# Kernel optimization log

Hardware: AMD Instinct MI355X
Metric: run time of the kernel (lower is better)

Reference implementation:

```python
import jax, jax.numpy as jnp
import numpy as np
from jax import lax

DIM = 384
HEADS = 8
HEAD_DIM = DIM // HEADS
MLP_HIDDEN = int(DIM * 4.0)
B, Hs, Ws = 32, 56, 56
N = Hs * Ws


def layernorm(x, w, b, eps=1e-5):
    mu = jnp.mean(x, axis=-1, keepdims=True)
    var = jnp.mean(jnp.square(x - mu), axis=-1, keepdims=True)
    return (x - mu) * lax.rsqrt(var + eps) * w + b


def setup_inputs() -> dict:
    key = jax.random.key(0)
    ks = jax.random.split(key, 16)
    s = 0.02
    inp = {
        "x": jax.random.normal(ks[0], (B, N, DIM), jnp.float32),
        "H": Hs,
        "W": Ws,
        # CPE depthwise 3x3 conv (groups=dim) -> OIHW kernel [C,1,3,3]
        "cpe_w": jax.random.normal(ks[1], (DIM, 1, 3, 3), jnp.float32) * s,
        "cpe_b": jnp.zeros((DIM,), jnp.float32),
        "ln1_w": jnp.ones((DIM,), jnp.float32),
        "ln1_b": jnp.zeros((DIM,), jnp.float32),
        "qkv_w": jax.random.normal(ks[2], (3 * DIM, DIM), jnp.float32) * s,
        "qkv_b": jnp.zeros((3 * DIM,), jnp.float32),
        "temperature": jnp.ones((HEADS, 1, 1), jnp.float32) * (HEAD_DIM ** -0.5),
        "proj_w": jax.random.normal(ks[3], (DIM, DIM), jnp.float32) * s,
        "proj_b": jnp.zeros((DIM,), jnp.float32),
        "ln2_w": jnp.ones((DIM,), jnp.float32),
        "ln2_b": jnp.zeros((DIM,), jnp.float32),
        "fc1_w": jax.random.normal(ks[4], (MLP_HIDDEN, DIM), jnp.float32) * s,
        "fc1_b": jnp.zeros((MLP_HIDDEN,), jnp.float32),
        "fc2_w": jax.random.normal(ks[5], (DIM, MLP_HIDDEN), jnp.float32) * s,
        "fc2_b": jnp.zeros((DIM,), jnp.float32),
    }
    return inp


def reference(x, H, W, cpe_w, cpe_b, ln1_w, ln1_b, qkv_w, qkv_b, temperature,
              proj_w, proj_b, ln2_w, ln2_b, fc1_w, fc1_b, fc2_w, fc2_b):
    Bn, Nn, C = x.shape
    # --- CPE: depthwise 3x3 conv residual (identity activation, cpe_act=False) ---
    feat = x.transpose(0, 2, 1).reshape(Bn, C, H, W)
    feat = lax.conv_general_dilated(
        feat, cpe_w, window_strides=(1, 1), padding="SAME",
        feature_group_count=C, dimension_numbers=("NCHW", "OIHW", "NCHW"))
    feat = feat + cpe_b[None, :, None, None]
    x = x + feat.reshape(Bn, C, Nn).transpose(0, 2, 1)

    # --- linear attention ---
    cur = layernorm(x, ln1_w, ln1_b)
    qkv = cur @ qkv_w.T + qkv_b                      # [B,N,3C]
    qkv = qkv.reshape(Bn, Nn, 3, HEADS, HEAD_DIM).transpose(2, 0, 3, 1, 4)
    q, k, v = qkv[0], qkv[1], qkv[2]                 # [B,h,N,d]
    q = jax.nn.relu(q)
    k = jax.nn.relu(k)
    k_sum = jnp.sum(k, axis=2)                       # [B,h,d]
    denom = jnp.maximum(jnp.einsum("bhnd,bhd->bhn", q, k_sum)[..., None], 100.0)
    kv = jnp.einsum("bhnd,bhne->bhde", k, v) * temperature  # [B,h,d,d]
    attn_out = jnp.einsum("bhnd,bhde->bhne", q, kv) / denom  # [B,h,N,d]
    attn_out = attn_out.transpose(0, 2, 1, 3).reshape(Bn, Nn, C)
    attn_out = attn_out @ proj_w.T + proj_b
    x = x + attn_out

    # --- MLP residual ---
    cur = layernorm(x, ln2_w, ln2_b)
    h = jax.nn.gelu(cur @ fc1_w.T + fc1_b, approximate=False)
    x = x + (h @ fc2_w.T + fc2_b)
    return x


if __name__ == "__main__":
    out = reference(**setup_inputs())
    print(out.shape, out.dtype)
```

## Files before the change

kernel.cpp:

```cpp
#include <hip/hip_runtime.h>
#include <hip/hip_bf16.h>
#include <math.h>

#define BDIM 384
#define HEADS 8
#define HD 48
#define HID 1536
#define BB 32
#define HH 56
#define WW 56
#define NN 3136
#define MTOT (BB*NN)
#define TPW 8

typedef unsigned short ushort_t;
typedef __attribute__((ext_vector_type(8))) short short8;
typedef __attribute__((ext_vector_type(4))) float floatx4;

__device__ inline float bf2f(ushort_t u){ return __uint_as_float(((unsigned)u)<<16); }
__device__ inline ushort_t f2bf(float f){
  unsigned u = __float_as_uint(f);
  u += 0x7fff + ((u>>16)&1);
  return (ushort_t)(u>>16);
}

__device__ inline void async_ld16(const void* g, void* l){
  __builtin_amdgcn_global_load_lds((const __attribute__((address_space(1))) void*)g,
                                   (__attribute__((address_space(3))) void*)l, 16, 0, 0);
}

__global__ void convert_bf16_kernel(const float* __restrict__ in, ushort_t* __restrict__ out, int n){
  int i = blockIdx.x*256 + threadIdx.x;
  if (i < n) out[i] = f2bf(in[i]);
}

__global__ __launch_bounds__(256)
void cpe_ln1_kernel(const float* __restrict__ x, const float* __restrict__ cw,
                    const float* __restrict__ cb, const float* __restrict__ lw,
                    const float* __restrict__ lb, float* __restrict__ x1out,
                    ushort_t* __restrict__ cur){
  int lane = threadIdx.x & 63, wave = threadIdx.x >> 6;
  size_t base = ((size_t)blockIdx.x*4 + wave) * TPW;
  float wreg[6][9], cbr[6], lwr[6], lbr[6];
  #pragma unroll
  for (int p = 0; p < 6; ++p){
    int c = p*64 + lane;
    cbr[p] = cb[c]; lwr[p] = lw[c]; lbr[p] = lb[c];
    #pragma unroll
    for (int j = 0; j < 9; ++j) wreg[p][j] = cw[c*9+j];
  }
  for (int ti = 0; ti < TPW; ++ti){
    size_t bn = base + ti;
    int b = (int)(bn / NN), n = (int)(bn % NN);
    int h = n / WW, w = n % WW;
    const float* xb = x + ((size_t)b*NN)*BDIM;
    float conv[6];
    #pragma unroll
    for (int p = 0; p < 6; ++p) conv[p] = cbr[p];
    #pragma unroll
    for (int dh = -1; dh <= 1; ++dh){
      int hh = h + dh; if ((unsigned)hh >= HH) continue;
      #pragma unroll
      for (int dw = -1; dw <= 1; ++dw){
        int w2 = w + dw; if ((unsigned)w2 >= WW) continue;
        const float* src = xb + (size_t)(hh*WW + w2)*BDIM + lane;
        int j = (dh+1)*3 + (dw+1);
        #pragma unroll
        for (int p = 0; p < 6; ++p) conv[p] += src[p*64] * wreg[p][j];
      }
    }
    const float* xc = xb + (size_t)n*BDIM + lane;
    float x1[6], s = 0.f, q = 0.f;
    #pragma unroll
    for (int p = 0; p < 6; ++p){
      x1[p] = xc[p*64] + conv[p];
      s += x1[p]; q += x1[p]*x1[p];
    }
    #pragma unroll
    for (int off = 32; off; off >>= 1){
      s += __shfl_xor(s, off);
      q += __shfl_xor(q, off);
    }
    float mean = s*(1.f/384.f);
    float rstd = rsqrtf(q*(1.f/384.f) - mean*mean + 1e-5f);
    float* xo = x1out + bn*BDIM + lane;
    ushort_t* co = cur + bn*BDIM + lane;
    #pragma unroll
    for (int p = 0; p < 6; ++p){
      xo[p*64] = x1[p];
      co[p*64] = f2bf((x1[p]-mean)*rstd*lwr[p] + lbr[p]);
    }
  }
}

__global__ __launch_bounds__(256)
void ln_kernel(const float* __restrict__ xin, const float* __restrict__ lw,
               const float* __restrict__ lb, ushort_t* __restrict__ outb){
  int lane = threadIdx.x & 63, wave = threadIdx.x >> 6;
  size_t base = ((size_t)blockIdx.x*4 + wave) * TPW;
  float lwr[6], lbr[6];
  #pragma unroll
  for (int p = 0; p < 6; ++p){ lwr[p] = lw[p*64+lane]; lbr[p] = lb[p*64+lane]; }
  for (int ti = 0; ti < TPW; ++ti){
    size_t bn = base + ti;
    const float* xi = xin + bn*BDIM + lane;
    float v[6], s = 0.f, q = 0.f;
    #pragma unroll
    for (int p = 0; p < 6; ++p){
      v[p] = xi[p*64];
      s += v[p]; q += v[p]*v[p];
    }
    #pragma unroll
    for (int off = 32; off; off >>= 1){
      s += __shfl_xor(s, off);
      q += __shfl_xor(q, off);
    }
    float mean = s*(1.f/384.f);
    float rstd = rsqrtf(q*(1.f/384.f) - mean*mean + 1e-5f);
    ushort_t* oo = outb + bn*BDIM + lane;
    #pragma unroll
    for (int p = 0; p < 6; ++p) oo[p*64] = f2bf((v[p]-mean)*rstd*lwr[p] + lbr[p]);
  }
}

template<int EP>
__global__ __launch_bounds__(256)
void gemm_kernel(const ushort_t* __restrict__ A, const ushort_t* __restrict__ Bw,
                 const float* __restrict__ bias, const float* __restrict__ resid,
                 void* __restrict__ outp, int Ncols, int K){
  __shared__ __align__(16) ushort_t As[2*128*32];
  __shared__ __align__(16) ushort_t Bs[2*128*32];
  const int t = threadIdx.x;
  const int lane = t & 63, wave = t >> 6;
  const int wm = wave >> 1, wn = wave & 1;

  const int gx = gridDim.x;
  const int nwg = gx * gridDim.y;
  int orig = blockIdx.y * gx + blockIdx.x;
  int qn = nwg >> 3, rn = nwg & 7;
  int xcd = orig & 7, pos = orig >> 3;
  int wg = (xcd < rn ? xcd*(qn+1) : rn*(qn+1) + (xcd-rn)*qn) + pos;
  int bx = wg % gx;
  int by = wg / gx;

  const size_t m0 = (size_t)by * 128;
  const int n0 = bx * 128;
  const int lrow = lane & 15, lk = (lane >> 4) << 3;
  floatx4 zero4 = {0.f, 0.f, 0.f, 0.f};
  floatx4 acc[4][4];
  #pragma unroll
  for (int i = 0; i < 4; ++i)
    #pragma unroll
    for (int j = 0; j < 4; ++j) acc[i][j] = zero4;

  for (int k0 = 0; k0 < K; k0 += 64){
    #pragma unroll
    for (int l = 0; l < 4; ++l){
      int idx = t + l*256;
      int row = (idx >> 2) & 127;
      int ko  = (idx >> 9)*32 + (idx & 3)*8;
      int lbase = (l*256 + wave*64) * 8;
      async_ld16(&A[(m0 + row)*K + (k0 + ko)], &As[lbase]);
      async_ld16(&Bw[(size_t)(n0 + row)*K + (k0 + ko)], &Bs[lbase]);
    }
    __syncthreads();
    #pragma unroll
    for (int half = 0; half < 2; ++half){
      const ushort_t* Ah = &As[half*4096];
      const ushort_t* Bh = &Bs[half*4096];
      short8 af[4], bfr[4];
      #pragma unroll
      for (int i = 0; i < 4; ++i) af[i]  = *(const short8*)&Ah[(wm*64 + i*16 + lrow)*32 + lk];
      #pragma unroll
      for (int j = 0; j < 4; ++j) bfr[j] = *(const short8*)&Bh[(wn*64 + j*16 + lrow)*32 + lk];
      #pragma unroll
      for (int i = 0; i < 4; ++i)
        #pragma unroll
        for (int j = 0; j < 4; ++j)
          acc[i][j] = __builtin_amdgcn_mfma_f32_16x16x32_bf16(af[i], bfr[j], acc[i][j], 0, 0, 0);
    }
    __syncthreads();
  }

  const int quad = lane >> 4;
  #pragma unroll
  for (int i = 0; i < 4; ++i){
    #pragma unroll
    for (int j = 0; j < 4; ++j){
      int gn = n0 + wn*64 + j*16 + lrow;
      float bv = bias[gn];
      #pragma unroll
      for (int r = 0; r < 4; ++r){
        size_t gm = m0 + wm*64 + i*16 + quad*4 + r;
        float v = acc[i][j][r] + bv;
        if constexpr (EP == 0){
          if (gn < 768) v = fmaxf(v, 0.f);
          ((ushort_t*)outp)[gm*Ncols + gn] = f2bf(v);
        } else if constexpr (EP == 1){
          v = 0.5f*v*(1.f + erff(v*0.70710678118f));
          ((ushort_t*)outp)[gm*Ncols + gn] = f2bf(v);
        } else {
          ((float*)outp)[gm*Ncols + gn] = v + resid[gm*Ncols + gn];
        }
      }
    }
  }
}

__global__ __launch_bounds__(256)
void kv_mfma_kernel(const ushort_t* __restrict__ qkv, float* __restrict__ kvT_out,
                    float* __restrict__ ksum_out){
  __shared__ __align__(16) ushort_t smem[2*48*72];
  ushort_t* kT = smem;
  ushort_t* vT = smem + 48*72;
  int bh = blockIdx.x, b = bh >> 3, h = bh & 7;
  int chunk = blockIdx.y;
  int t = threadIdx.x, lane = t & 63, wave = t >> 6;
  int lrow = lane & 15, quad = lane >> 4;
  const ushort_t* kb = qkv + (size_t)b*NN*1152 + 384 + h*48;
  const ushort_t* vb = kb + 384;
  floatx4 acc[9];
  #pragma unroll
  for (int i = 0; i < 9; ++i) acc[i] = (floatx4){0.f,0.f,0.f,0.f};
  float ks = 0.f;

  for (int s = 0; s < 7; ++s){
    int n0 = chunk*448 + s*64;
    #pragma unroll
    for (int p = 0; p < 3; ++p){
      int u = t + p*256;
      int arr = u / 384;
      int r = u - arr*384;
      int d8 = r >> 6;
      int nl = r & 63;
      const ushort_t* src = (arr ? vb : kb) + (size_t)(n0 + nl)*1152 + d8*8;
      ushort_t* dst = arr ? vT : kT;
      uint4 val = *(const uint4*)src;
      ushort_t tmp[8];
      *(uint4*)tmp = val;
      #pragma unroll
      for (int j = 0; j < 8; ++j) dst[(d8*8 + j)*72 + nl] = tmp[j];
    }
    __syncthreads();
    if ((wave >> 1) == (s & 1)){
      int kloc = (wave & 1) * 32;
      short8 af[3], bfv[3];
      #pragma unroll
      for (int i = 0; i < 3; ++i) af[i]  = *(const short8*)&kT[(i*16 + lrow)*72 + kloc + quad*8];
      #pragma unroll
      for (int j = 0; j < 3; ++j) bfv[j] = *(const short8*)&vT[(j*16 + lrow)*72 + kloc + quad*8];
      #pragma unroll
      for (int i = 0; i < 3; ++i)
        #pragma unroll
        for (int j = 0; j < 3; ++j)
          acc[i*3+j] = __builtin_amdgcn_mfma_f32_16x16x32_bf16(af[i], bfv[j], acc[i*3+j], 0, 0, 0);
    }
    if (wave == 3 && lane < 48){
      float s2 = 0.f;
      #pragma unroll
      for (int q8 = 0; q8 < 8; ++q8){
        short8 kk = *(const short8*)&kT[lane*72 + q8*8];
        #pragma unroll
        for (int j = 0; j < 8; ++j) s2 += bf2f((ushort_t)kk[j]);
      }
      ks += s2;
    }
    __syncthreads();
  }

  float* F = (float*)smem;
  #define DUMP(W) if (wave == (W)){ _Pragma("unroll") for (int ti = 0; ti < 9; ++ti){ _Pragma("unroll") for (int r = 0; r < 4; ++r){ int d = (ti/3)*16 + quad*4 + r, e = (ti%3)*16 + lrow; F[d*48 + e] = acc[ti][r]; } } }
  #define ADDF(W) if (wave == (W)){ _Pragma("unroll") for (int ti = 0; ti < 9; ++ti){ _Pragma("unroll") for (int r = 0; r < 4; ++r){ int d = (ti/3)*16 + quad*4 + r, e = (ti%3)*16 + lrow; acc[ti][r] += F[d*48 + e]; } } }
  DUMP(1) __syncthreads(); ADDF(0) __syncthreads();
  DUMP(3) __syncthreads(); ADDF(2) __syncthreads();
  DUMP(2) __syncthreads(); ADDF(0) __syncthreads();
  #undef DUMP
  #undef ADDF
  if (wave == 0){
    #pragma unroll
    for (int ti = 0; ti < 9; ++ti){
      #pragma unroll
      for (int r = 0; r < 4; ++r){
        int d = (ti/3)*16 + quad*4 + r, e = (ti%3)*16 + lrow;
        atomicAdd(&kvT_out[(size_t)bh*2304 + e*48 + d], acc[ti][r]);
      }
    }
  }
  if (wave == 3 && lane < 48) atomicAdd(&ksum_out[bh*48 + lane], ks);
}

__global__ __launch_bounds__(256)
void attn_mfma_kernel(const ushort_t* __restrict__ qkv, const float* __restrict__ kvT,
                      const float* __restrict__ ksum, const float* __restrict__ temp,
                      ushort_t* __restrict__ attn_out){
  __shared__ __align__(16) ushort_t Bs[64*72];
  int bh = blockIdx.x, b = bh >> 3, h = bh & 7;
  int t = threadIdx.x, lane = t & 63, wave = t >> 6;
  int lrow = lane & 15, quad = lane >> 4;
  float tf = temp[h];
  for (int u = t; u < 64*72; u += 256){
    int col = u / 72, d = u - col*72;
    float v = 0.f;
    if (d < 48){
      if (col < 48) v = kvT[(size_t)bh*2304 + col*48 + d] * tf;
      else if (col == 48) v = ksum[bh*48 + d];
    }
    Bs[u] = f2bf(v);
  }
  __syncthreads();
  short8 bfv[4][2];
  #pragma unroll
  for (int j = 0; j < 4; ++j)
    #pragma unroll
    for (int s = 0; s < 2; ++s)
      bfv[j][s] = *(const short8*)&Bs[(j*16 + lrow)*72 + s*32 + quad*8];

  const ushort_t* qb = qkv + (size_t)b*NN*1152 + h*48;
  int n0 = blockIdx.y*256 + wave*64;
  floatx4 acc[4][4];
  #pragma unroll
  for (int i = 0; i < 4; ++i)
    #pragma unroll
    for (int j = 0; j < 4; ++j) acc[i][j] = (floatx4){0.f,0.f,0.f,0.f};

  #pragma unroll
  for (int i = 0; i < 4; ++i){
    int nrow = n0 + i*16 + lrow;
    #pragma unroll
    for (int s = 0; s < 2; ++s){
      short8 af = *(const short8*)&qb[(size_t)nrow*1152 + s*32 + quad*8];
      #pragma unroll
      for (int j = 0; j < 4; ++j)
        acc[i][j] = __builtin_amdgcn_mfma_f32_16x16x32_bf16(af, bfv[j][s], acc[i][j], 0, 0, 0);
    }
  }

  ushort_t* ob = attn_out + (size_t)b*NN*BDIM + h*48;
  #pragma unroll
  for (int i = 0; i < 4; ++i){
    #pragma unroll
    for (int r = 0; r < 4; ++r){
      float den = __shfl(acc[i][3][r], quad*16);
      den = fmaxf(den, 100.f);
      int nrow = n0 + i*16 + quad*4 + r;
      if (nrow < NN){
        #pragma unroll
        for (int j = 0; j < 3; ++j)
          ob[(size_t)nrow*BDIM + j*16 + lrow] = f2bf(acc[i][j][r] / den);
      }
    }
  }
}

extern "C" void kernel_launch(void* const* d_in, const int* in_sizes, int n_in,
                              void* d_out, int out_size, void* d_ws, size_t ws_size,
                              hipStream_t stream){
  const float* x     = (const float*)d_in[0];
  const float* cpe_w = (const float*)d_in[3];
  const float* cpe_b = (const float*)d_in[4];
  const float* ln1_w = (const float*)d_in[5];
  const float* ln1_b = (const float*)d_in[6];
  const float* qkv_w = (const float*)d_in[7];
  const float* qkv_b = (const float*)d_in[8];
  const float* temp  = (const float*)d_in[9];
  const float* proj_w= (const float*)d_in[10];
  const float* proj_b= (const float*)d_in[11];
  const float* ln2_w = (const float*)d_in[12];
  const float* ln2_b = (const float*)d_in[13];
  const float* fc1_w = (const float*)d_in[14];
  const float* fc1_b = (const float*)d_in[15];
  const float* fc2_w = (const float*)d_in[16];
  const float* fc2_b = (const float*)d_in[17];
  float* out = (float*)d_out;

  char* ws = (char*)d_ws;
  size_t off = 0;
  auto alloc = [&](size_t bytes) -> void* {
    void* p = ws + off;
    off += (bytes + 255) & ~(size_t)255;
    return p;
  };
  ushort_t* cur  = (ushort_t*)alloc((size_t)MTOT*BDIM*2);
  ushort_t* big  = (ushort_t*)alloc((size_t)MTOT*HID*2);
  float*    kvT  = (float*)   alloc((size_t)BB*HEADS*HD*HD*4);
  float*    ksum = (float*)   alloc((size_t)BB*HEADS*HD*4);
  ushort_t* wq = (ushort_t*)alloc((size_t)3*BDIM*BDIM*2);
  ushort_t* wp = (ushort_t*)alloc((size_t)BDIM*BDIM*2);
  ushort_t* w1 = (ushort_t*)alloc((size_t)HID*BDIM*2);
  ushort_t* w2 = (ushort_t*)alloc((size_t)BDIM*HID*2);

  convert_bf16_kernel<<<(3*BDIM*BDIM + 255)/256, 256, 0, stream>>>(qkv_w, wq, 3*BDIM*BDIM);
  convert_bf16_kernel<<<(BDIM*BDIM + 255)/256, 256, 0, stream>>>(proj_w, wp, BDIM*BDIM);
  convert_bf16_kernel<<<(HID*BDIM + 255)/256, 256, 0, stream>>>(fc1_w, w1, HID*BDIM);
  convert_bf16_kernel<<<(BDIM*HID + 255)/256, 256, 0, stream>>>(fc2_w, w2, BDIM*HID);

  hipMemsetAsync(kvT, 0, (size_t)BB*HEADS*HD*HD*4, stream);
  hipMemsetAsync(ksum, 0, (size_t)BB*HEADS*HD*4, stream);

  cpe_ln1_kernel<<<MTOT/(4*TPW), 256, 0, stream>>>(x, cpe_w, cpe_b, ln1_w, ln1_b, out, cur);
  gemm_kernel<0><<<dim3(9, 784), 256, 0, stream>>>(cur, wq, qkv_b, nullptr, big, 1152, BDIM);
  kv_mfma_kernel<<<dim3(BB*HEADS, 7), 256, 0, stream>>>(big, kvT, ksum);
  attn_mfma_kernel<<<dim3(BB*HEADS, 13), 256, 0, stream>>>(big, kvT, ksum, temp, cur);
  gemm_kernel<2><<<dim3(3, 784), 256, 0, stream>>>(cur, wp, proj_b, out, out, BDIM, BDIM);
  ln_kernel<<<MTOT/(4*TPW), 256, 0, stream>>>(out, ln2_w, ln2_b, cur);
  gemm_kernel<1><<<dim3(12, 784), 256, 0, stream>>>(cur, w1, fc1_b, nullptr, big, HID, BDIM);
  gemm_kernel<2><<<dim3(3, 784), 256, 0, stream>>>(big, w2, fc2_b, out, out, BDIM, HID);
}
```

Measured before the change: 1.419 ms.

## Enlarge GEMM tile to 256 rows with 512 threads and use fast erf

The GEMM block tile grows from 128x128 to 256x128, using 8 waves and 512 threads, so each weight tile in LDS is shared by twice as many rows and the number of blocks halves. The exact erff in the GELU epilogue is replaced by the Abramowitz-Stegun polynomial approximation built on exp2f, which lowers epilogue arithmetic at a small accuracy cost (max error around 1e-7). The larger tile uses more LDS per block, which may cut occupancy, and it leaves fewer blocks to spread across the CUs.

```diff
diff --git a/kernel.cpp b/kernel.cpp
--- a/kernel.cpp
+++ b/kernel.cpp
@@ -24,6 +24,16 @@
   return (ushort_t)(u>>16);
 }
 
+__device__ inline float erf_fast(float z){
+  float az = fabsf(z);
+  float tt = 1.f/(1.f + 0.3275911f*az);
+  float poly = tt*(0.254829592f + tt*(-0.284496736f + tt*(1.421413741f +
+               tt*(-1.453152027f + tt*1.061405429f))));
+  float e = exp2f(-az*az*1.4426950408889634f);
+  float r = 1.f - poly*e;
+  return copysignf(r, z);
+}
+
 __device__ inline void async_ld16(const void* g, void* l){
   __builtin_amdgcn_global_load_lds((const __attribute__((address_space(1))) void*)g,
                                    (__attribute__((address_space(3))) void*)l, 16, 0, 0);
@@ -124,11 +134,11 @@
 }
 
 template<int EP>
-__global__ __launch_bounds__(256)
+__global__ __launch_bounds__(512)
 void gemm_kernel(const ushort_t* __restrict__ A, const ushort_t* __restrict__ Bw,
                  const float* __restrict__ bias, const float* __restrict__ resid,
                  void* __restrict__ outp, int Ncols, int K){
-  __shared__ __align__(16) ushort_t As[2*128*32];
+  __shared__ __align__(16) ushort_t As[2*256*32];
   __shared__ __align__(16) ushort_t Bs[2*128*32];
   const int t = threadIdx.x;
   const int lane = t & 63, wave = t >> 6;
@@ -143,7 +153,7 @@
   int bx = wg % gx;
   int by = wg / gx;
 
-  const size_t m0 = (size_t)by * 128;
+  const size_t m0 = (size_t)by * 256;
   const int n0 = bx * 128;
   const int lrow = lane & 15, lk = (lane >> 4) << 3;
   floatx4 zero4 = {0.f, 0.f, 0.f, 0.f};
@@ -156,17 +166,21 @@
   for (int k0 = 0; k0 < K; k0 += 64){
     #pragma unroll
     for (int l = 0; l < 4; ++l){
-      int idx = t + l*256;
-      int row = (idx >> 2) & 127;
-      int ko  = (idx >> 9)*32 + (idx & 3)*8;
-      int lbase = (l*256 + wave*64) * 8;
-      async_ld16(&A[(m0 + row)*K + (k0 + ko)], &As[lbase]);
-      async_ld16(&Bw[(size_t)(n0 + row)*K + (k0 + ko)], &Bs[lbase]);
+      int idx = t + l*512;
+      int lbase = (l*512 + wave*64) * 8;
+      int arow = (idx >> 2) & 255;
+      int ako  = (idx >> 10)*32 + (idx & 3)*8;
+      async_ld16(&A[(m0 + arow)*K + (k0 + ako)], &As[lbase]);
+      if (l < 2){
+        int brow = (idx >> 2) & 127;
+        int bko  = (idx >> 9)*32 + (idx & 3)*8;
+        async_ld16(&Bw[(size_t)(n0 + brow)*K + (k0 + bko)], &Bs[lbase]);
+      }
     }
     __syncthreads();
     #pragma unroll
     for (int half = 0; half < 2; ++half){
-      const ushort_t* Ah = &As[half*4096];
+      const ushort_t* Ah = &As[half*8192];
       const ushort_t* Bh = &Bs[half*4096];
       short8 af[4], bfr[4];
       #pragma unroll
@@ -197,7 +211,7 @@
           if (gn < 768) v = fmaxf(v, 0.f);
           ((ushort_t*)outp)[gm*Ncols + gn] = f2bf(v);
         } else if constexpr (EP == 1){
-          v = 0.5f*v*(1.f + erff(v*0.70710678118f));
+          v = 0.5f*v*(1.f + erf_fast(v*0.70710678118f));
           ((ushort_t*)outp)[gm*Ncols + gn] = f2bf(v);
         } else {
           ((float*)outp)[gm*Ncols + gn] = v + resid[gm*Ncols + gn];
@@ -398,11 +412,11 @@
   hipMemsetAsync(ksum, 0, (size_t)BB*HEADS*HD*4, stream);
 
   cpe_ln1_kernel<<<MTOT/(4*TPW), 256, 0, stream>>>(x, cpe_w, cpe_b, ln1_w, ln1_b, out, cur);
-  gemm_kernel<0><<<dim3(9, 784), 256, 0, stream>>>(cur, wq, qkv_b, nullptr, big, 1152, BDIM);
+  gemm_kernel<0><<<dim3(9, MTOT/256), 512, 0, stream>>>(cur, wq, qkv_b, nullptr, big, 1152, BDIM);
   kv_mfma_kernel<<<dim3(BB*HEADS, 7), 256, 0, stream>>>(big, kvT, ksum);
   attn_mfma_kernel<<<dim3(BB*HEADS, 13), 256, 0, stream>>>(big, kvT, ksum, temp, cur);
-  gemm_kernel<2><<<dim3(3, 784), 256, 0, stream>>>(cur, wp, proj_b, out, out, BDIM, BDIM);
+  gemm_kernel<2><<<dim3(3, MTOT/256), 512, 0, stream>>>(cur, wp, proj_b, out, out, BDIM, BDIM);
   ln_kernel<<<MTOT/(4*TPW), 256, 0, stream>>>(out, ln2_w, ln2_b, cur);
-  gemm_kernel<1><<<dim3(12, 784), 256, 0, stream>>>(cur, w1, fc1_b, nullptr, big, HID, BDIM);
-  gemm_kernel<2><<<dim3(3, 784), 256, 0, stream>>>(big, w2, fc2_b, out, out, BDIM, HID);
-}
+  gemm_kernel<1><<<dim3(12, MTOT/256), 512, 0, stream>>>(cur, w1, fc1_b, nullptr, big, HID, BDIM);
+  gemm_kernel<2><<<dim3(3, MTOT/256), 512, 0, stream>>>(big, w2, fc2_b, out, out, BDIM, HID);
+}
```

Result: no change. 1.399 ms (-1.4%).
